# Optimization experiments

Hardware: AMD Instinct MI355X
Metric: run time of the kernel (lower is better)

## Reference

```python
import jax, jax.numpy as jnp
import numpy as np

NEIGH = (3, 3, 3)  # attn_neighbourhood_size -> 27 one-hot impulse filters


def setup_inputs() -> dict:
    key = jax.random.key(0)
    b, h, d = 2, 8, 32
    H = W = D = 24
    x = jax.random.normal(key, (b, h, H * W * D, d), dtype=jnp.float32)
    return {"x": x, "height": H, "width": W, "depth": D}


def _localize(x, height, width, depth):
    # x: [b, h, N, d] with N = height*width*depth
    b, h, N, d = x.shape
    nh, nw, nd = NEIGH
    ph, pw, pd = (nh - 1) // 2, (nw - 1) // 2, (nd - 1) // 2
    # 'b h (i j k) d -> b h d i j k'
    y = x.reshape(b, h, height, width, depth, d).transpose(0, 1, 5, 2, 3, 4)
    yp = jnp.pad(y, ((0, 0), (0, 0), (0, 0), (ph, ph), (pw, pw), (pd, pd)))
    # conv3d with a unit impulse at (i,j,k) and 'same' padding is exactly the
    # shifted gather out[p] = x_padded[p + (i,j,k)]; emit the 27 shifts directly.
    slices = []
    for i in range(nh):
        for j in range(nw):
            for k in range(nd):
                slices.append(yp[..., i:i + height, j:j + width, k:k + depth])
    # [b, h, d, H, W, D, filter_n]
    out = jnp.stack(slices, axis=-1)
    fn = nh * nw * nd
    # '(b h d) filter_n i j k -> b h (i j k) filter_n d'
    out = out.reshape(b, h, d, N, fn).transpose(0, 1, 3, 4, 2)
    return out


def reference(x, height, width, depth):
    return _localize(x, height, width, depth)
```

## Files before the change

### kernel.cpp

```cpp
#include <hip/hip_runtime.h>


typedef float v4f __attribute__((ext_vector_type(4)));

constexpr int H = 24, W = 24, D = 24;
constexpr int N = H * W * D;
constexpr int FN = 27;
constexpr int BH = 16;
constexpr int PLEN = D + 2;
constexpr int LDS_N4 = 9 * PLEN * 8;
constexpr int OUT_N4 = D * FN * 8;

__global__ __launch_bounds__(256) void localize_kernel(
    const v4f* __restrict__ x4, v4f* __restrict__ out4) {
  __shared__ v4f lds[LDS_N4];
  const int tid = threadIdx.x;
  const int wg  = blockIdx.x;
  const int bh  = wg / (H * W);
  const int rem = wg - bh * (H * W);
  const int ii  = rem / W;
  const int jj  = rem - ii * W;

  for (int o = tid; o < LDS_N4; o += 256) {
    int c4   = o & 7;
    int r    = o >> 3;
    int p    = r / PLEN;
    int srck = r - p * PLEN;
    int si   = ii + p / 3 - 1;
    int sj   = jj + p % 3 - 1;
    int sk   = srck - 1;
    v4f v = (v4f)(0.0f);
    if ((unsigned)si < (unsigned)H && (unsigned)sj < (unsigned)W &&
        (unsigned)sk < (unsigned)D) {
      v = x4[(((bh * H + si) * W + sj) * D + sk) * 8 + c4];
    }
    lds[o] = v;
  }
  __syncthreads();

  const int base = (bh * N + ii * (W * D) + jj * D) * (FN * 8);
  for (int o = tid; o < OUT_N4; o += 256) {
    int c4   = o & 7;
    int t    = o >> 3;
    int f    = t % FN;
    int kk   = t / FN;
    int p    = f / 3;
    int srck = kk + f % 3;
    v4f v = lds[(p * PLEN + srck) * 8 + c4];
    __builtin_nontemporal_store(v, &out4[base + o]);
  }
}

extern "C" void kernel_launch(void* const* d_in, const int* in_sizes, int n_in,
                              void* d_out, int out_size, void* d_ws, size_t ws_size,
                              hipStream_t stream) {
  (void)in_sizes; (void)n_in; (void)out_size; (void)d_ws; (void)ws_size;
  const v4f* x4 = (const v4f*)d_in[0];
  v4f* out4 = (v4f*)d_out;
  int blocks = BH * H * W;
  localize_kernel<<<blocks, 256, 0, stream>>>(x4, out4);
}
```

Measured before the change: 758.6 us.

## Use direct global-to-LDS loads, 576-thread blocks, and swizzled block order

The load phase now issues async global_load_lds DMA copies into LDS, one wave per neighbour row, and zeroes halo or out-of-range rows with explicit stores. Blocks grow to 576 threads so the output loop runs exactly 9 iterations, with incremental index updates that replace the per-element div/mod. Block IDs are remapped in strides of one eighth of the grid to spread work across XCDs. The aim is to cut index arithmetic and load latency in this store-bound copy kernel. The risks are lower occupancy from the larger blocks and correctness concerns around how the LDS DMA completes relative to the barrier.

```diff
diff --git a/kernel.cpp b/kernel.cpp
--- a/kernel.cpp
+++ b/kernel.cpp
@@ -2,52 +2,76 @@
 
 
 typedef float v4f __attribute__((ext_vector_type(4)));
+typedef const __attribute__((address_space(1))) v4f* gptr_t;
+typedef __attribute__((address_space(3))) v4f* lptr_t;
 
 constexpr int H = 24, W = 24, D = 24;
 constexpr int N = H * W * D;
 constexpr int FN = 27;
 constexpr int BH = 16;
 constexpr int PLEN = D + 2;
-constexpr int LDS_N4 = 9 * PLEN * 8;
-constexpr int OUT_N4 = D * FN * 8;
+constexpr int P_N4 = PLEN * 8;
+constexpr int LDS_N4 = 9 * P_N4;
+constexpr int NT = 576;
+constexpr int NWG = BH * H * W;
 
-__global__ __launch_bounds__(256) void localize_kernel(
+__global__ __launch_bounds__(NT) void localize_kernel(
     const v4f* __restrict__ x4, v4f* __restrict__ out4) {
   __shared__ v4f lds[LDS_N4];
-  const int tid = threadIdx.x;
-  const int wg  = blockIdx.x;
+  const int tid  = threadIdx.x;
+  const int lane = tid & 63;
+  const int wv   = tid >> 6;
+
+  const int bid = blockIdx.x;
+  const int wg  = (bid & 7) * (NWG / 8) + (bid >> 3);
+
   const int bh  = wg / (H * W);
   const int rem = wg - bh * (H * W);
   const int ii  = rem / W;
   const int jj  = rem - ii * W;
 
-  for (int o = tid; o < LDS_N4; o += 256) {
-    int c4   = o & 7;
-    int r    = o >> 3;
-    int p    = r / PLEN;
-    int srck = r - p * PLEN;
-    int si   = ii + p / 3 - 1;
-    int sj   = jj + p % 3 - 1;
-    int sk   = srck - 1;
-    v4f v = (v4f)(0.0f);
-    if ((unsigned)si < (unsigned)H && (unsigned)sj < (unsigned)W &&
-        (unsigned)sk < (unsigned)D) {
-      v = x4[(((bh * H + si) * W + sj) * D + sk) * 8 + c4];
+  const int pdi = wv / 3;
+  const int si  = ii + pdi - 1;
+  const int sj  = jj + (wv - pdi * 3) - 1;
+  const int pbase = wv * P_N4;
+
+  if ((unsigned)si < (unsigned)H && (unsigned)sj < (unsigned)W) {
+    if (lane < 16) {
+      int off = (lane < 8) ? lane : (25 * 8 + (lane - 8));
+      lds[pbase + off] = (v4f)(0.0f);
     }
-    lds[o] = v;
+    const v4f* g = x4 + (((bh * H + si) * W + sj) * D) * 8;
+#pragma unroll
+    for (int it = 0; it < 3; ++it) {
+      const v4f* gp = g + it * 64 + lane;
+      v4f* lp = &lds[pbase + 8 + it * 64];
+      __builtin_amdgcn_global_load_lds((gptr_t)gp, (lptr_t)lp, 16, 0, 0);
+    }
+  } else {
+#pragma unroll
+    for (int it = 0; it < 4; ++it) {
+      int off = it * 64 + lane;
+      if (off < P_N4) lds[pbase + off] = (v4f)(0.0f);
+    }
   }
   __syncthreads();
 
-  const int base = (bh * N + ii * (W * D) + jj * D) * (FN * 8);
-  for (int o = tid; o < OUT_N4; o += 256) {
-    int c4   = o & 7;
-    int t    = o >> 3;
-    int f    = t % FN;
-    int kk   = t / FN;
-    int p    = f / 3;
-    int srck = kk + f % 3;
-    v4f v = lds[(p * PLEN + srck) * 8 + c4];
-    __builtin_nontemporal_store(v, &out4[base + o]);
+  const int c4 = tid & 7;
+  int t  = tid >> 3;
+  int kk = t / FN;
+  int f  = t - kk * FN;
+  int p  = f / 3;
+  const int fm3 = f - p * 3;
+  int ldsidx = (p * PLEN + kk + fm3) * 8 + c4;
+  const int base = (bh * N + ii * (W * D) + jj * D) * (FN * 8) + tid;
+#pragma unroll
+  for (int i = 0; i < 9; ++i) {
+    v4f v = lds[ldsidx];
+    __builtin_nontemporal_store(v, &out4[base + i * NT]);
+    p += 6;
+    int drow = 158;
+    if (p >= 9) { p -= 9; drow = -75; }
+    ldsidx += drow * 8;
   }
 }
 
@@ -57,6 +81,5 @@
   (void)in_sizes; (void)n_in; (void)out_size; (void)d_ws; (void)ws_size;
   const v4f* x4 = (const v4f*)d_in[0];
   v4f* out4 = (v4f*)d_out;
-  int blocks = BH * H * W;
-  localize_kernel<<<blocks, 256, 0, stream>>>(x4, out4);
+  localize_kernel<<<NWG, NT, 0, stream>>>(x4, out4);
 }
```

Measured after the change: 762.7 us. Within noise of the previous version (+0.5%).
